# Performance work log

Hardware: AMD Instinct MI355X
Metric: run time of the kernel (lower is better)

The kernel has to match this reference:

```python
import jax, jax.numpy as jnp
import numpy as np

N = 16384
D = 512
NNZ = 163840
NUM_ITERS = 10


def setup_inputs() -> dict:
    key = jax.random.key(0)
    k1, k2, k3, k4 = jax.random.split(key, 4)
    x = jax.random.normal(k1, (N, D), dtype=jnp.float32)
    edge_val = jax.random.uniform(k2, (NNZ,), dtype=jnp.float32)
    edge_row = jnp.sort(jax.random.randint(k3, (NNZ,), 0, N, dtype=jnp.int32))
    edge_col = jax.random.randint(k4, (NNZ,), 0, N, dtype=jnp.int32)
    alpha = jnp.zeros((1,), dtype=jnp.float32)
    beta = jnp.zeros((1,), dtype=jnp.float32)
    sigma = jnp.ones((1,), dtype=jnp.float32)
    return {"x": x, "alpha": alpha, "beta": beta, "sigma": sigma,
            "edge_val": edge_val, "edge_row": edge_row, "edge_col": edge_col,
            "num_iters": NUM_ITERS}


def reference(x, alpha, beta, sigma, edge_val, edge_row, edge_col, num_iters):
    n = x.shape[0]
    # tf.nn.l2_normalize(x, axis=1)
    xn = x * jax.lax.rsqrt(jnp.maximum(jnp.sum(x * x, axis=1, keepdims=True), 1e-12))
    # cosine similarity only at sparse support positions; diagonal zeroed
    sim_e = jnp.sum(xn[edge_row] * xn[edge_col], axis=-1)          # [nnz]
    sim_e = jnp.where(edge_row == edge_col, 0.0, sim_e)
    s = jnp.exp(sigma[0])
    sigma_sq = 2.0 * s * s
    sim_e = jnp.exp(sim_e / (2.0 * sigma_sq))
    # support = sparse support elementwise * similarity
    sup = edge_val * sim_e                                          # [nnz]
    # row-sum of sparse support
    normalize = jax.ops.segment_sum(sup, edge_row, num_segments=n)  # [N]
    a = jnp.exp(alpha[0])
    b = jnp.exp(beta[0])
    denom = b + normalize[:, None] * a + a                          # [N,1] -> broadcast over D

    def step(out, _):
        # sparse matmul: (support @ out)
        Ax = jax.ops.segment_sum(sup[:, None] * out[edge_col], edge_row, num_segments=n)
        out = (x * b + (Ax + out) * a) / denom
        return out, None

    out, _ = jax.lax.scan(step, x, None, length=num_iters)
    return out
```

## Files before the change

kernel.cpp:

```cpp
#include <hip/hip_runtime.h>
#include <hip/hip_fp16.h>

#define DIM 512
#define N_ITERS 10

typedef float floatx2 __attribute__((ext_vector_type(2)));

__device__ __forceinline__ unsigned int pack2h(float lo, float hi) {
    __half2 h = __float22half2_rn(make_float2(lo, hi));
    return *reinterpret_cast<unsigned int*>(&h);
}
__device__ __forceinline__ float2 unpack2h(unsigned int u) {
    return __half22float2(*reinterpret_cast<__half2*>(&u));
}
__device__ __forceinline__ unsigned int pack4f8(float f0, float f1, float f2, float f3) {
    int v = 0;
    v = __builtin_amdgcn_cvt_pk_fp8_f32(f0, f1, v, false);
    v = __builtin_amdgcn_cvt_pk_fp8_f32(f2, f3, v, true);
    return (unsigned int)v;
}

__global__ void consts_kernel(const float* alpha, const float* beta,
                              const float* sigma, float* consts) {
    if (threadIdx.x == 0 && blockIdx.x == 0) {
        float a = expf(alpha[0]);
        float b = expf(beta[0]);
        float s = expf(sigma[0]);
        consts[0] = a;
        consts[1] = b;
        consts[2] = 1.0f / (4.0f * s * s);
    }
}

__global__ void __launch_bounds__(256)
rownorm_kernel(const float* __restrict__ x,
               const float* __restrict__ consts,
               unsigned short* __restrict__ xh16,
               unsigned int* __restrict__ x8,
               unsigned int* __restrict__ xn8,
               unsigned short* __restrict__ xbh, int n) {
    int wid = (blockIdx.x * blockDim.x + threadIdx.x) >> 6;
    int lane = threadIdx.x & 63;
    if (wid >= n) return;
    const size_t base = (size_t)wid * DIM + lane * 8;
    const float4* p = (const float4*)(x + base);
    float4 u = p[0];
    float4 v = p[1];
    float s = u.x*u.x + u.y*u.y + u.z*u.z + u.w*u.w
            + v.x*v.x + v.y*v.y + v.z*v.z + v.w*v.w;
    uint4 h;
    h.x = pack2h(u.x, u.y); h.y = pack2h(u.z, u.w);
    h.z = pack2h(v.x, v.y); h.w = pack2h(v.z, v.w);
    *(uint4*)(xh16 + base) = h;
    uint2 q;
    q.x = pack4f8(u.x, u.y, u.z, u.w);
    q.y = pack4f8(v.x, v.y, v.z, v.w);
    *(uint2*)(x8 + ((size_t)wid * (DIM / 4) + lane * 2)) = q;
    float b = consts[1];
    uint4 hb;
    hb.x = pack2h(u.x * b, u.y * b); hb.y = pack2h(u.z * b, u.w * b);
    hb.z = pack2h(v.x * b, v.y * b); hb.w = pack2h(v.z * b, v.w * b);
    *(uint4*)(xbh + base) = hb;
    #pragma unroll
    for (int m = 32; m >= 1; m >>= 1) s += __shfl_xor(s, m, 64);
    float inr = rsqrtf(fmaxf(s, 1e-12f));
    uint2 qn;
    qn.x = pack4f8(u.x * inr, u.y * inr, u.z * inr, u.w * inr);
    qn.y = pack4f8(v.x * inr, v.y * inr, v.z * inr, v.w * inr);
    *(uint2*)(xn8 + ((size_t)wid * (DIM / 4) + lane * 2)) = qn;
}

__global__ void rowptr_kernel(const int* __restrict__ erow, int nnz,
                              int* __restrict__ rstart, int n) {
    int r = blockIdx.x * blockDim.x + threadIdx.x;
    if (r > n) return;
    int lo = 0, hi = nnz;
    while (lo < hi) {
        int mid = (lo + hi) >> 1;
        if (erow[mid] < r) lo = mid + 1; else hi = mid;
    }
    rstart[r] = lo;
}

__device__ __forceinline__ float dot8f8(const float* A, uint2 h) {
    floatx2 p0 = __builtin_amdgcn_cvt_pk_f32_fp8((int)h.x, false);
    floatx2 p1 = __builtin_amdgcn_cvt_pk_f32_fp8((int)h.x, true);
    floatx2 p2 = __builtin_amdgcn_cvt_pk_f32_fp8((int)h.y, false);
    floatx2 p3 = __builtin_amdgcn_cvt_pk_f32_fp8((int)h.y, true);
    return A[0]*p0.x + A[1]*p0.y + A[2]*p1.x + A[3]*p1.y
         + A[4]*p2.x + A[5]*p2.y + A[6]*p3.x + A[7]*p3.y;
}

__global__ void __launch_bounds__(256)
edge_row_kernel(const unsigned int* __restrict__ xn8,
                const float* __restrict__ eval_,
                const int* __restrict__ ecol,
                const int* __restrict__ rstart,
                const float* __restrict__ consts,
                float* __restrict__ sup, float* __restrict__ inv_denom, int n) {
    int row = (blockIdx.x * blockDim.x + threadIdx.x) >> 6;
    int lane = threadIdx.x & 63;
    if (row >= n) return;
    uint2 hr = *(const uint2*)(xn8 + (size_t)row * (DIM / 4) + lane * 2);
    float A[8];
    {
        floatx2 p0 = __builtin_amdgcn_cvt_pk_f32_fp8((int)hr.x, false);
        floatx2 p1 = __builtin_amdgcn_cvt_pk_f32_fp8((int)hr.x, true);
        floatx2 p2 = __builtin_amdgcn_cvt_pk_f32_fp8((int)hr.y, false);
        floatx2 p3 = __builtin_amdgcn_cvt_pk_f32_fp8((int)hr.y, true);
        A[0]=p0.x; A[1]=p0.y; A[2]=p1.x; A[3]=p1.y;
        A[4]=p2.x; A[5]=p2.y; A[6]=p3.x; A[7]=p3.y;
    }
    float c2 = consts[2];
    int rs = rstart[row], re = rstart[row + 1];
    float norm_acc = 0.0f;
    int e = rs;
    for (; e + 3 < re; e += 4) {
        int c[4]; uint2 h[4]; float s[4];
        #pragma unroll
        for (int j = 0; j < 4; ++j) c[j] = ecol[e + j];
        #pragma unroll
        for (int j = 0; j < 4; ++j)
            h[j] = *(const uint2*)(xn8 + (size_t)c[j] * (DIM / 4) + lane * 2);
        #pragma unroll
        for (int j = 0; j < 4; ++j) s[j] = dot8f8(A, h[j]);
        #pragma unroll
        for (int m = 32; m >= 1; m >>= 1) {
            #pragma unroll
            for (int j = 0; j < 4; ++j) s[j] += __shfl_xor(s[j], m, 64);
        }
        #pragma unroll
        for (int j = 0; j < 4; ++j) {
            float sim = (row == c[j]) ? 0.0f : s[j];
            float sp = eval_[e + j] * expf(sim * c2);
            norm_acc += sp;
            if (lane == 0) sup[e + j] = sp;
        }
    }
    for (; e < re; ++e) {
        int c0 = ecol[e];
        uint2 h0 = *(const uint2*)(xn8 + (size_t)c0 * (DIM / 4) + lane * 2);
        float s0 = dot8f8(A, h0);
        #pragma unroll
        for (int m = 32; m >= 1; m >>= 1) s0 += __shfl_xor(s0, m, 64);
        float sim0 = (row == c0) ? 0.0f : s0;
        float sp0 = eval_[e] * expf(sim0 * c2);
        norm_acc += sp0;
        if (lane == 0) sup[e] = sp0;
    }
    if (lane == 0) {
        float a = consts[0], b = consts[1];
        inv_denom[row] = 1.0f / (b + norm_acc * a + a);
    }
}

#define ACCF8(hh, ww)                                                              \
    do {                                                                           \
        floatx2 p_;                                                                \
        p_ = __builtin_amdgcn_cvt_pk_f32_fp8((int)(hh).x, false); acc0 += (ww)*p_.x; acc1 += (ww)*p_.y; \
        p_ = __builtin_amdgcn_cvt_pk_f32_fp8((int)(hh).x, true);  acc2 += (ww)*p_.x; acc3 += (ww)*p_.y; \
        p_ = __builtin_amdgcn_cvt_pk_f32_fp8((int)(hh).y, false); acc4 += (ww)*p_.x; acc5 += (ww)*p_.y; \
        p_ = __builtin_amdgcn_cvt_pk_f32_fp8((int)(hh).y, true);  acc6 += (ww)*p_.x; acc7 += (ww)*p_.y; \
    } while (0)

__global__ void __launch_bounds__(256)
iter_kernel(const unsigned short* __restrict__ prev16,
            const unsigned int* __restrict__ prev8,
            unsigned short* __restrict__ next16,
            unsigned int* __restrict__ next8,
            float* __restrict__ out_f32, int last,
            const float* __restrict__ consts, const float* __restrict__ inv_denom,
            const float* __restrict__ sup, const int* __restrict__ ecol,
            const int* __restrict__ rstart,
            const unsigned short* __restrict__ xbh, int n) {
    int row = (blockIdx.x * blockDim.x + threadIdx.x) >> 6;
    int lane = threadIdx.x & 63;
    if (row >= n) return;
    float a = consts[0];
    float inv_d = inv_denom[row];
    int rs = rstart[row], re = rstart[row + 1];
    const size_t loff16 = lane * 8;
    const size_t base16 = (size_t)row * DIM + loff16;
    const size_t loff8 = lane * 2;
    float acc0 = 0.f, acc1 = 0.f, acc2 = 0.f, acc3 = 0.f;
    float acc4 = 0.f, acc5 = 0.f, acc6 = 0.f, acc7 = 0.f;
    int e = rs;
    for (; e + 7 < re; e += 8) {
        int c[8]; float w[8]; uint2 h[8];
        #pragma unroll
        for (int j = 0; j < 8; ++j) { c[j] = ecol[e + j]; w[j] = sup[e + j]; }
        #pragma unroll
        for (int j = 0; j < 8; ++j)
            h[j] = *(const uint2*)(prev8 + (size_t)c[j] * (DIM / 4) + loff8);
        #pragma unroll
        for (int j = 0; j < 8; ++j) ACCF8(h[j], w[j]);
    }
    for (; e + 1 < re; e += 2) {
        int c0 = ecol[e], c1 = ecol[e + 1];
        float w0 = sup[e], w1 = sup[e + 1];
        uint2 h0 = *(const uint2*)(prev8 + (size_t)c0 * (DIM / 4) + loff8);
        uint2 h1 = *(const uint2*)(prev8 + (size_t)c1 * (DIM / 4) + loff8);
        ACCF8(h0, w0);
        ACCF8(h1, w1);
    }
    if (e < re) {
        float w = sup[e];
        int c = ecol[e];
        uint2 h = *(const uint2*)(prev8 + (size_t)c * (DIM / 4) + loff8);
        ACCF8(h, w);
    }
    uint4 hs = *(const uint4*)(prev16 + base16);
    uint4 hx = *(const uint4*)(xbh + base16);
    float2 s0 = unpack2h(hs.x), s1 = unpack2h(hs.y);
    float2 s2 = unpack2h(hs.z), s3 = unpack2h(hs.w);
    float2 x0 = unpack2h(hx.x), x1 = unpack2h(hx.y);
    float2 x2 = unpack2h(hx.z), x3 = unpack2h(hx.w);
    float r0 = (x0.x + (acc0 + s0.x) * a) * inv_d;
    float r1 = (x0.y + (acc1 + s0.y) * a) * inv_d;
    float r2 = (x1.x + (acc2 + s1.x) * a) * inv_d;
    float r3 = (x1.y + (acc3 + s1.y) * a) * inv_d;
    float r4 = (x2.x + (acc4 + s2.x) * a) * inv_d;
    float r5 = (x2.y + (acc5 + s2.y) * a) * inv_d;
    float r6 = (x3.x + (acc6 + s3.x) * a) * inv_d;
    float r7 = (x3.y + (acc7 + s3.y) * a) * inv_d;
    if (last) {
        float4* o = (float4*)(out_f32 + base16);
        o[0] = make_float4(r0, r1, r2, r3);
        o[1] = make_float4(r4, r5, r6, r7);
    } else {
        uint4 ho;
        ho.x = pack2h(r0, r1); ho.y = pack2h(r2, r3);
        ho.z = pack2h(r4, r5); ho.w = pack2h(r6, r7);
        *(uint4*)(next16 + base16) = ho;
        uint2 q;
        q.x = pack4f8(r0, r1, r2, r3);
        q.y = pack4f8(r4, r5, r6, r7);
        *(uint2*)(next8 + (size_t)row * (DIM / 4) + loff8) = q;
    }
}

extern "C" void kernel_launch(void* const* d_in, const int* in_sizes, int n_in,
                              void* d_out, int out_size, void* d_ws, size_t ws_size,
                              hipStream_t stream) {
    const float* x     = (const float*)d_in[0];
    const float* alpha = (const float*)d_in[1];
    const float* beta  = (const float*)d_in[2];
    const float* sigma = (const float*)d_in[3];
    const float* eval_ = (const float*)d_in[4];
    const int* erow = (const int*)d_in[5];
    const int* ecol = (const int*)d_in[6];

    const int n   = in_sizes[0] / DIM;
    const int nnz = in_sizes[4];

    float* ws        = (float*)d_ws;
    float* consts    = ws;
    float* inv_denom = ws + 64;
    int*   rstart    = (int*)(inv_denom + n);
    float* sup       = (float*)(rstart + n + 64);
    unsigned short* xbh   = (unsigned short*)(sup + nnz);
    unsigned short* bufB16= xbh + (size_t)n * DIM;
    unsigned int*   xn8   = (unsigned int*)(bufB16 + (size_t)n * DIM);
    unsigned int*   bufA8 = xn8 + (size_t)n * (DIM / 4);
    unsigned int*   bufB8 = bufA8 + (size_t)n * (DIM / 4);
    unsigned short* bufA16 = (unsigned short*)d_out;
    float* out_f32 = (float*)d_out;

    consts_kernel<<<1, 64, 0, stream>>>(alpha, beta, sigma, consts);
    rownorm_kernel<<<(n * 64) / 256, 256, 0, stream>>>(x, consts, bufA16, bufA8, xn8, xbh, n);
    rowptr_kernel<<<(n + 256) / 256, 256, 0, stream>>>(erow, nnz, rstart, n);
    edge_row_kernel<<<(n * 64) / 256, 256, 0, stream>>>(xn8, eval_, ecol,
                                                        rstart, consts,
                                                        sup, inv_denom, n);

    for (int it = 0; it < N_ITERS; ++it) {
        const unsigned short* prev16 = (it & 1) ? bufB16 : bufA16;
        const unsigned int*   prev8  = (it & 1) ? bufB8  : bufA8;
        unsigned short* next16 = (it & 1) ? bufA16 : bufB16;
        unsigned int*   next8  = (it & 1) ? bufA8  : bufB8;
        int last = (it == N_ITERS - 1) ? 1 : 0;
        iter_kernel<<<(n * 64) / 256, 256, 0, stream>>>(prev16, prev8, next16, next8,
                                                        out_f32, last,
                                                        consts, inv_denom, sup, ecol,
                                                        rstart, xbh, n);
    }
}
```

Baseline: 331.6 us.

## Fuse first propagation iteration into edge-similarity kernel with interleaved fp8 rows

Rownorm now writes one interleaved fp8 buffer per row holding both the normalized and raw values, so a single 16-byte gather serves the similarity dot and the first SpMM step. The edge kernel computes each edge weight and immediately accumulates the first iteration's output, which removes one full iteration launch and one gather pass. Accumulators are switched to packed float2 FMAs, and nontemporal loads and stores are applied to streamed buffers. The trade-off is a wider per-edge gather in the fused kernel and a buffer layout that aliases bufA8 with the interleaved array.

```diff
diff --git a/kernel.cpp b/kernel.cpp
--- a/kernel.cpp
+++ b/kernel.cpp
@@ -5,6 +5,8 @@
 #define N_ITERS 10
 
 typedef float floatx2 __attribute__((ext_vector_type(2)));
+typedef float fx4 __attribute__((ext_vector_type(4)));
+typedef unsigned int ux4 __attribute__((ext_vector_type(4)));
 
 __device__ __forceinline__ unsigned int pack2h(float lo, float hi) {
     __half2 h = __float22half2_rn(make_float2(lo, hi));
@@ -35,39 +37,31 @@
 __global__ void __launch_bounds__(256)
 rownorm_kernel(const float* __restrict__ x,
                const float* __restrict__ consts,
-               unsigned short* __restrict__ xh16,
-               unsigned int* __restrict__ x8,
-               unsigned int* __restrict__ xn8,
+               unsigned int* __restrict__ xc8,
                unsigned short* __restrict__ xbh, int n) {
     int wid = (blockIdx.x * blockDim.x + threadIdx.x) >> 6;
     int lane = threadIdx.x & 63;
     if (wid >= n) return;
     const size_t base = (size_t)wid * DIM + lane * 8;
-    const float4* p = (const float4*)(x + base);
-    float4 u = p[0];
-    float4 v = p[1];
+    const fx4* p = (const fx4*)(x + base);
+    fx4 u = __builtin_nontemporal_load(p);
+    fx4 v = __builtin_nontemporal_load(p + 1);
     float s = u.x*u.x + u.y*u.y + u.z*u.z + u.w*u.w
             + v.x*v.x + v.y*v.y + v.z*v.z + v.w*v.w;
-    uint4 h;
-    h.x = pack2h(u.x, u.y); h.y = pack2h(u.z, u.w);
-    h.z = pack2h(v.x, v.y); h.w = pack2h(v.z, v.w);
-    *(uint4*)(xh16 + base) = h;
-    uint2 q;
-    q.x = pack4f8(u.x, u.y, u.z, u.w);
-    q.y = pack4f8(v.x, v.y, v.z, v.w);
-    *(uint2*)(x8 + ((size_t)wid * (DIM / 4) + lane * 2)) = q;
     float b = consts[1];
-    uint4 hb;
+    ux4 hb;
     hb.x = pack2h(u.x * b, u.y * b); hb.y = pack2h(u.z * b, u.w * b);
     hb.z = pack2h(v.x * b, v.y * b); hb.w = pack2h(v.z * b, v.w * b);
-    *(uint4*)(xbh + base) = hb;
+    *(ux4*)(xbh + base) = hb;
     #pragma unroll
     for (int m = 32; m >= 1; m >>= 1) s += __shfl_xor(s, m, 64);
     float inr = rsqrtf(fmaxf(s, 1e-12f));
-    uint2 qn;
-    qn.x = pack4f8(u.x * inr, u.y * inr, u.z * inr, u.w * inr);
-    qn.y = pack4f8(v.x * inr, v.y * inr, v.z * inr, v.w * inr);
-    *(uint2*)(xn8 + ((size_t)wid * (DIM / 4) + lane * 2)) = qn;
+    ux4 q;
+    q.x = pack4f8(u.x * inr, u.y * inr, u.z * inr, u.w * inr);
+    q.y = pack4f8(v.x * inr, v.y * inr, v.z * inr, v.w * inr);
+    q.z = pack4f8(u.x, u.y, u.z, u.w);
+    q.w = pack4f8(v.x, v.y, v.z, v.w);
+    *(ux4*)(xc8 + ((size_t)wid * 256 + lane * 4)) = q;
 }
 
 __global__ void rowptr_kernel(const int* __restrict__ erow, int nnz,
@@ -82,26 +76,37 @@
     rstart[r] = lo;
 }
 
-__device__ __forceinline__ float dot8f8(const float* A, uint2 h) {
-    floatx2 p0 = __builtin_amdgcn_cvt_pk_f32_fp8((int)h.x, false);
-    floatx2 p1 = __builtin_amdgcn_cvt_pk_f32_fp8((int)h.x, true);
-    floatx2 p2 = __builtin_amdgcn_cvt_pk_f32_fp8((int)h.y, false);
-    floatx2 p3 = __builtin_amdgcn_cvt_pk_f32_fp8((int)h.y, true);
+__device__ __forceinline__ float dot8f8(const float* A, unsigned int lo, unsigned int hi) {
+    floatx2 p0 = __builtin_amdgcn_cvt_pk_f32_fp8((int)lo, false);
+    floatx2 p1 = __builtin_amdgcn_cvt_pk_f32_fp8((int)lo, true);
+    floatx2 p2 = __builtin_amdgcn_cvt_pk_f32_fp8((int)hi, false);
+    floatx2 p3 = __builtin_amdgcn_cvt_pk_f32_fp8((int)hi, true);
     return A[0]*p0.x + A[1]*p0.y + A[2]*p1.x + A[3]*p1.y
          + A[4]*p2.x + A[5]*p2.y + A[6]*p3.x + A[7]*p3.y;
 }
 
+#define ACCP(lo, hi, w2)                                                          \
+    do {                                                                          \
+        acc0 += (w2) * __builtin_amdgcn_cvt_pk_f32_fp8((int)(lo), false);         \
+        acc1 += (w2) * __builtin_amdgcn_cvt_pk_f32_fp8((int)(lo), true);          \
+        acc2 += (w2) * __builtin_amdgcn_cvt_pk_f32_fp8((int)(hi), false);         \
+        acc3 += (w2) * __builtin_amdgcn_cvt_pk_f32_fp8((int)(hi), true);          \
+    } while (0)
+
 __global__ void __launch_bounds__(256)
-edge_row_kernel(const unsigned int* __restrict__ xn8,
-                const float* __restrict__ eval_,
-                const int* __restrict__ ecol,
-                const int* __restrict__ rstart,
-                const float* __restrict__ consts,
-                float* __restrict__ sup, float* __restrict__ inv_denom, int n) {
+fused1_kernel(const unsigned int* __restrict__ xc8,
+              const float* __restrict__ x,
+              const float* __restrict__ eval_,
+              const int* __restrict__ ecol,
+              const int* __restrict__ rstart,
+              const float* __restrict__ consts,
+              float* __restrict__ sup, float* __restrict__ inv_denom,
+              unsigned short* __restrict__ next16,
+              unsigned int* __restrict__ next8, int n) {
     int row = (blockIdx.x * blockDim.x + threadIdx.x) >> 6;
     int lane = threadIdx.x & 63;
     if (row >= n) return;
-    uint2 hr = *(const uint2*)(xn8 + (size_t)row * (DIM / 4) + lane * 2);
+    ux4 hr = *(const ux4*)(xc8 + (size_t)row * 256 + lane * 4);
     float A[8];
     {
         floatx2 p0 = __builtin_amdgcn_cvt_pk_f32_fp8((int)hr.x, false);
@@ -111,19 +116,20 @@
         A[0]=p0.x; A[1]=p0.y; A[2]=p1.x; A[3]=p1.y;
         A[4]=p2.x; A[5]=p2.y; A[6]=p3.x; A[7]=p3.y;
     }
-    float c2 = consts[2];
+    float a = consts[0], b = consts[1], c2 = consts[2];
     int rs = rstart[row], re = rstart[row + 1];
     float norm_acc = 0.0f;
+    floatx2 acc0 = {0.f, 0.f}, acc1 = {0.f, 0.f}, acc2 = {0.f, 0.f}, acc3 = {0.f, 0.f};
     int e = rs;
     for (; e + 3 < re; e += 4) {
-        int c[4]; uint2 h[4]; float s[4];
-        #pragma unroll
-        for (int j = 0; j < 4; ++j) c[j] = ecol[e + j];
+        int c[4]; float ev[4]; ux4 h[4]; float s[4];
+        #pragma unroll
+        for (int j = 0; j < 4; ++j) { c[j] = ecol[e + j]; ev[j] = eval_[e + j]; }
         #pragma unroll
         for (int j = 0; j < 4; ++j)
-            h[j] = *(const uint2*)(xn8 + (size_t)c[j] * (DIM / 4) + lane * 2);
-        #pragma unroll
-        for (int j = 0; j < 4; ++j) s[j] = dot8f8(A, h[j]);
+            h[j] = *(const ux4*)(xc8 + (size_t)c[j] * 256 + lane * 4);
+        #pragma unroll
+        for (int j = 0; j < 4; ++j) s[j] = dot8f8(A, h[j].x, h[j].y);
         #pragma unroll
         for (int m = 32; m >= 1; m >>= 1) {
             #pragma unroll
@@ -132,36 +138,50 @@
         #pragma unroll
         for (int j = 0; j < 4; ++j) {
             float sim = (row == c[j]) ? 0.0f : s[j];
-            float sp = eval_[e + j] * expf(sim * c2);
+            float sp = ev[j] * expf(sim * c2);
             norm_acc += sp;
             if (lane == 0) sup[e + j] = sp;
+            floatx2 w2 = {sp, sp};
+            ACCP(h[j].z, h[j].w, w2);
         }
     }
     for (; e < re; ++e) {
         int c0 = ecol[e];
-        uint2 h0 = *(const uint2*)(xn8 + (size_t)c0 * (DIM / 4) + lane * 2);
-        float s0 = dot8f8(A, h0);
+        float ev0 = eval_[e];
+        ux4 h0 = *(const ux4*)(xc8 + (size_t)c0 * 256 + lane * 4);
+        float s0 = dot8f8(A, h0.x, h0.y);
         #pragma unroll
         for (int m = 32; m >= 1; m >>= 1) s0 += __shfl_xor(s0, m, 64);
         float sim0 = (row == c0) ? 0.0f : s0;
-        float sp0 = eval_[e] * expf(sim0 * c2);
+        float sp0 = ev0 * expf(sim0 * c2);
         norm_acc += sp0;
         if (lane == 0) sup[e] = sp0;
-    }
-    if (lane == 0) {
-        float a = consts[0], b = consts[1];
-        inv_denom[row] = 1.0f / (b + norm_acc * a + a);
-    }
-}
-
-#define ACCF8(hh, ww)                                                              \
-    do {                                                                           \
-        floatx2 p_;                                                                \
-        p_ = __builtin_amdgcn_cvt_pk_f32_fp8((int)(hh).x, false); acc0 += (ww)*p_.x; acc1 += (ww)*p_.y; \
-        p_ = __builtin_amdgcn_cvt_pk_f32_fp8((int)(hh).x, true);  acc2 += (ww)*p_.x; acc3 += (ww)*p_.y; \
-        p_ = __builtin_amdgcn_cvt_pk_f32_fp8((int)(hh).y, false); acc4 += (ww)*p_.x; acc5 += (ww)*p_.y; \
-        p_ = __builtin_amdgcn_cvt_pk_f32_fp8((int)(hh).y, true);  acc6 += (ww)*p_.x; acc7 += (ww)*p_.y; \
-    } while (0)
+        floatx2 w2 = {sp0, sp0};
+        ACCP(h0.z, h0.w, w2);
+    }
+    float inv_d = 1.0f / (b + norm_acc * a + a);
+    if (lane == 0) inv_denom[row] = inv_d;
+    const size_t base = (size_t)row * DIM + lane * 8;
+    const fx4* px = (const fx4*)(x + base);
+    fx4 u = __builtin_nontemporal_load(px);
+    fx4 v = __builtin_nontemporal_load(px + 1);
+    float r0 = (u.x * b + (acc0.x + u.x) * a) * inv_d;
+    float r1 = (u.y * b + (acc0.y + u.y) * a) * inv_d;
+    float r2 = (u.z * b + (acc1.x + u.z) * a) * inv_d;
+    float r3 = (u.w * b + (acc1.y + u.w) * a) * inv_d;
+    float r4 = (v.x * b + (acc2.x + v.x) * a) * inv_d;
+    float r5 = (v.y * b + (acc2.y + v.y) * a) * inv_d;
+    float r6 = (v.z * b + (acc3.x + v.z) * a) * inv_d;
+    float r7 = (v.w * b + (acc3.y + v.w) * a) * inv_d;
+    ux4 ho;
+    ho.x = pack2h(r0, r1); ho.y = pack2h(r2, r3);
+    ho.z = pack2h(r4, r5); ho.w = pack2h(r6, r7);
+    __builtin_nontemporal_store(ho, (ux4*)(next16 + base));
+    uint2 q;
+    q.x = pack4f8(r0, r1, r2, r3);
+    q.y = pack4f8(r4, r5, r6, r7);
+    *(uint2*)(next8 + (size_t)row * (DIM / 4) + lane * 2) = q;
+}
 
 __global__ void __launch_bounds__(256)
 iter_kernel(const unsigned short* __restrict__ prev16,
@@ -182,8 +202,7 @@
     const size_t loff16 = lane * 8;
     const size_t base16 = (size_t)row * DIM + loff16;
     const size_t loff8 = lane * 2;
-    float acc0 = 0.f, acc1 = 0.f, acc2 = 0.f, acc3 = 0.f;
-    float acc4 = 0.f, acc5 = 0.f, acc6 = 0.f, acc7 = 0.f;
+    floatx2 acc0 = {0.f, 0.f}, acc1 = {0.f, 0.f}, acc2 = {0.f, 0.f}, acc3 = {0.f, 0.f};
     int e = rs;
     for (; e + 7 < re; e += 8) {
         int c[8]; float w[8]; uint2 h[8];
@@ -193,45 +212,50 @@
         for (int j = 0; j < 8; ++j)
             h[j] = *(const uint2*)(prev8 + (size_t)c[j] * (DIM / 4) + loff8);
         #pragma unroll
-        for (int j = 0; j < 8; ++j) ACCF8(h[j], w[j]);
+        for (int j = 0; j < 8; ++j) {
+            floatx2 w2 = {w[j], w[j]};
+            ACCP(h[j].x, h[j].y, w2);
+        }
     }
     for (; e + 1 < re; e += 2) {
         int c0 = ecol[e], c1 = ecol[e + 1];
         float w0 = sup[e], w1 = sup[e + 1];
         uint2 h0 = *(const uint2*)(prev8 + (size_t)c0 * (DIM / 4) + loff8);
         uint2 h1 = *(const uint2*)(prev8 + (size_t)c1 * (DIM / 4) + loff8);
-        ACCF8(h0, w0);
-        ACCF8(h1, w1);
+        floatx2 w20 = {w0, w0}; ACCP(h0.x, h0.y, w20);
+        floatx2 w21 = {w1, w1}; ACCP(h1.x, h1.y, w21);
     }
     if (e < re) {
         float w = sup[e];
         int c = ecol[e];
         uint2 h = *(const uint2*)(prev8 + (size_t)c * (DIM / 4) + loff8);
-        ACCF8(h, w);
-    }
-    uint4 hs = *(const uint4*)(prev16 + base16);
-    uint4 hx = *(const uint4*)(xbh + base16);
+        floatx2 w2 = {w, w}; ACCP(h.x, h.y, w2);
+    }
+    ux4 hs = __builtin_nontemporal_load((const ux4*)(prev16 + base16));
+    ux4 hx = __builtin_nontemporal_load((const ux4*)(xbh + base16));
     float2 s0 = unpack2h(hs.x), s1 = unpack2h(hs.y);
     float2 s2 = unpack2h(hs.z), s3 = unpack2h(hs.w);
     float2 x0 = unpack2h(hx.x), x1 = unpack2h(hx.y);
     float2 x2 = unpack2h(hx.z), x3 = unpack2h(hx.w);
-    float r0 = (x0.x + (acc0 + s0.x) * a) * inv_d;
-    float r1 = (x0.y + (acc1 + s0.y) * a) * inv_d;
-    float r2 = (x1.x + (acc2 + s1.x) * a) * inv_d;
-    float r3 = (x1.y + (acc3 + s1.y) * a) * inv_d;
-    float r4 = (x2.x + (acc4 + s2.x) * a) * inv_d;
-    float r5 = (x2.y + (acc5 + s2.y) * a) * inv_d;
-    float r6 = (x3.x + (acc6 + s3.x) * a) * inv_d;
-    float r7 = (x3.y + (acc7 + s3.y) * a) * inv_d;
+    float r0 = (x0.x + (acc0.x + s0.x) * a) * inv_d;
+    float r1 = (x0.y + (acc0.y + s0.y) * a) * inv_d;
+    float r2 = (x1.x + (acc1.x + s1.x) * a) * inv_d;
+    float r3 = (x1.y + (acc1.y + s1.y) * a) * inv_d;
+    float r4 = (x2.x + (acc2.x + s2.x) * a) * inv_d;
+    float r5 = (x2.y + (acc2.y + s2.y) * a) * inv_d;
+    float r6 = (x3.x + (acc3.x + s3.x) * a) * inv_d;
+    float r7 = (x3.y + (acc3.y + s3.y) * a) * inv_d;
     if (last) {
-        float4* o = (float4*)(out_f32 + base16);
-        o[0] = make_float4(r0, r1, r2, r3);
-        o[1] = make_float4(r4, r5, r6, r7);
+        fx4* o = (fx4*)(out_f32 + base16);
+        fx4 o0 = {r0, r1, r2, r3};
+        fx4 o1 = {r4, r5, r6, r7};
+        __builtin_nontemporal_store(o0, o);
+        __builtin_nontemporal_store(o1, o + 1);
     } else {
-        uint4 ho;
+        ux4 ho;
         ho.x = pack2h(r0, r1); ho.y = pack2h(r2, r3);
         ho.z = pack2h(r4, r5); ho.w = pack2h(r6, r7);
-        *(uint4*)(next16 + base16) = ho;
+        __builtin_nontemporal_store(ho, (ux4*)(next16 + base16));
         uint2 q;
         q.x = pack4f8(r0, r1, r2, r3);
         q.y = pack4f8(r4, r5, r6, r7);
@@ -258,27 +282,26 @@
     float* inv_denom = ws + 64;
     int*   rstart    = (int*)(inv_denom + n);
     float* sup       = (float*)(rstart + n + 64);
-    unsigned short* xbh   = (unsigned short*)(sup + nnz);
-    unsigned short* bufB16= xbh + (size_t)n * DIM;
-    unsigned int*   xn8   = (unsigned int*)(bufB16 + (size_t)n * DIM);
-    unsigned int*   bufA8 = xn8 + (size_t)n * (DIM / 4);
-    unsigned int*   bufB8 = bufA8 + (size_t)n * (DIM / 4);
+    unsigned short* xbh    = (unsigned short*)(sup + nnz);
+    unsigned short* bufB16 = xbh + (size_t)n * DIM;
+    unsigned int*   xc8    = (unsigned int*)(bufB16 + (size_t)n * DIM);
+    unsigned int*   bufB8  = xc8 + (size_t)n * 256;
+    unsigned int*   bufA8  = xc8;
     unsigned short* bufA16 = (unsigned short*)d_out;
     float* out_f32 = (float*)d_out;
 
     consts_kernel<<<1, 64, 0, stream>>>(alpha, beta, sigma, consts);
-    rownorm_kernel<<<(n * 64) / 256, 256, 0, stream>>>(x, consts, bufA16, bufA8, xn8, xbh, n);
+    rownorm_kernel<<<(n * 64) / 256, 256, 0, stream>>>(x, consts, xc8, xbh, n);
     rowptr_kernel<<<(n + 256) / 256, 256, 0, stream>>>(erow, nnz, rstart, n);
-    edge_row_kernel<<<(n * 64) / 256, 256, 0, stream>>>(xn8, eval_, ecol,
-                                                        rstart, consts,
-                                                        sup, inv_denom, n);
-
-    for (int it = 0; it < N_ITERS; ++it) {
-        const unsigned short* prev16 = (it & 1) ? bufB16 : bufA16;
-        const unsigned int*   prev8  = (it & 1) ? bufB8  : bufA8;
-        unsigned short* next16 = (it & 1) ? bufA16 : bufB16;
-        unsigned int*   next8  = (it & 1) ? bufA8  : bufB8;
-        int last = (it == N_ITERS - 1) ? 1 : 0;
+    fused1_kernel<<<(n * 64) / 256, 256, 0, stream>>>(xc8, x, eval_, ecol, rstart,
+                                                      consts, sup, inv_denom,
+                                                      bufB16, bufB8, n);
+    for (int k = 0; k < N_ITERS - 1; ++k) {
+        const unsigned short* prev16 = (k & 1) ? bufA16 : bufB16;
+        const unsigned int*   prev8  = (k & 1) ? bufA8  : bufB8;
+        unsigned short* next16 = (k & 1) ? bufB16 : bufA16;
+        unsigned int*   next8  = (k & 1) ? bufB8  : bufA8;
+        int last = (k == N_ITERS - 2) ? 1 : 0;
         iter_kernel<<<(n * 64) / 256, 256, 0, stream>>>(prev16, prev8, next16, next8,
                                                         out_f32, last,
                                                         consts, inv_denom, sup, ecol,
```

Result: slower. 344.2 us (+3.8%).
